# Kernel optimization log

Measured on AMD Instinct MI355X. Metric: run time of the kernel, lower is better.

The kernel has to match this reference:

```python
import jax, jax.numpy as jnp
import numpy as np

NUM_BITS_ACTS = 8
NUM_BITS_PARAMS = 8
NUM_BITS_ACCUM = 32


def quantized_range(num_bits):
    # distiller-style signed range: [-2^(n-1), 2^(n-1)-1]
    n = 2.0 ** num_bits
    return -n / 2.0, n / 2.0 - 1.0


def sym_scale(num_bits, sat_abs):
    # scale = (2^(n-1)-1) / max_abs
    return (2.0 ** (num_bits - 1) - 1.0) / sat_abs


def quant_clamp(t, scale, qmin, qmax):
    return jnp.clip(jnp.round(t * scale), qmin, qmax)


def setup_inputs() -> dict:
    key = jax.random.key(0)
    kx, kw = jax.random.split(key)
    x = jax.random.normal(kx, (8192, 4096), dtype=jnp.float32)
    W = jax.random.normal(kw, (4096, 4096), dtype=jnp.float32)  # [out, in]
    return {"x": x, "W": W}


def reference(x, W):
    acts_min, acts_max = quantized_range(NUM_BITS_ACTS)
    params_min, params_max = quantized_range(NUM_BITS_PARAMS)
    accum_min, accum_max = quantized_range(NUM_BITS_ACCUM)

    # __init__: quantize weights once (symmetric, max-abs)
    w_scale = sym_scale(NUM_BITS_PARAMS, jnp.max(jnp.abs(W)))
    W_q = quant_clamp(W, w_scale, params_min, params_max)

    # pre_quantized_forward: input scale from max-abs, quantize-clamp input
    in_scale = sym_scale(NUM_BITS_ACTS, jnp.max(jnp.abs(x)))
    x_q = quant_clamp(x, in_scale, acts_min, acts_max)

    # wrapped Linear in integer domain, clamp to accumulator range
    accum = jnp.clip(x_q @ W_q.T, accum_min, accum_max)  # [8192, 4096]

    # post_quantized_forward: requantize accumulator to output range
    accum_scale = in_scale * w_scale
    accum_max_abs = jnp.max(jnp.abs(accum))
    y_f_max_abs = accum_max_abs / accum_scale
    out_scale = sym_scale(NUM_BITS_ACTS, y_f_max_abs)
    requant_scale = out_scale / accum_scale

    out_q = quant_clamp(accum, requant_scale, acts_min, acts_max)
    out_f = out_q / out_scale  # dequantize
    return out_f
```

## Files before the change

kernel.cpp:

```cpp
#include <hip/hip_runtime.h>
#include <stdint.h>


using i32x4 = __attribute__((ext_vector_type(4))) int;

#define M_DIM 8192
#define N_DIM 4096
#define K_DIM 4096

#define BM 128
#define BN 128
#define BK 128

__global__ void k_init(unsigned* sc) {
    sc[0] = 0u;
    sc[1] = 0u;
    sc[2] = 0u;
}

__global__ __launch_bounds__(256) void k_absmax(const float4* __restrict__ src, int n4,
                                                unsigned* __restrict__ out) {
    unsigned m = 0;
    int stride = gridDim.x * blockDim.x;
    for (int i = blockIdx.x * blockDim.x + threadIdx.x; i < n4; i += stride) {
        float4 v = src[i];
        unsigned a = __float_as_uint(v.x) & 0x7fffffffu;
        unsigned b = __float_as_uint(v.y) & 0x7fffffffu;
        unsigned c = __float_as_uint(v.z) & 0x7fffffffu;
        unsigned d = __float_as_uint(v.w) & 0x7fffffffu;
        m = max(m, max(max(a, b), max(c, d)));
    }
    for (int off = 32; off; off >>= 1)
        m = max(m, (unsigned)__shfl_xor((int)m, off));
    __shared__ unsigned wm[4];
    int ln = threadIdx.x & 63, wv = threadIdx.x >> 6;
    if (ln == 0) wm[wv] = m;
    __syncthreads();
    if (threadIdx.x == 0)
        atomicMax(out, max(max(wm[0], wm[1]), max(wm[2], wm[3])));
}

__global__ __launch_bounds__(256) void k_quant(const float4* __restrict__ src,
                                               unsigned* __restrict__ dst, int n4,
                                               const unsigned* __restrict__ maxbits) {
    float scale = 127.0f / __uint_as_float(*maxbits);
    int stride = gridDim.x * blockDim.x;
    for (int i = blockIdx.x * blockDim.x + threadIdx.x; i < n4; i += stride) {
        float4 v = src[i];
        int q0 = min(127, max(-128, (int)rintf(v.x * scale)));
        int q1 = min(127, max(-128, (int)rintf(v.y * scale)));
        int q2 = min(127, max(-128, (int)rintf(v.z * scale)));
        int q3 = min(127, max(-128, (int)rintf(v.w * scale)));
        dst[i] = (unsigned)(q0 & 0xff) | ((unsigned)(q1 & 0xff) << 8) |
                 ((unsigned)(q2 & 0xff) << 16) | ((unsigned)(q3 & 0xff) << 24);
    }
}

__global__ __launch_bounds__(256) void k_gemm(const char* __restrict__ Aq,
                                              const char* __restrict__ Bq,
                                              int* __restrict__ C,
                                              unsigned* __restrict__ maxAcc) {
    __shared__ char lA[BM * BK];
    __shared__ char lB[BN * BK];

    const int bx = blockIdx.x;
    const int by = blockIdx.y;
    const int t  = threadIdx.x;
    const int ln = t & 63;
    const int wv = t >> 6;
    const int wr  = wv >> 1;
    const int wcl = wv & 1;
    const int lr = ln & 15;
    const int lk = ln >> 4;

    i32x4 acc[4][4];
#pragma unroll
    for (int i = 0; i < 4; ++i)
#pragma unroll
        for (int j = 0; j < 4; ++j) acc[i][j] = (i32x4)(0);

    const size_t arow0 = (size_t)by * BM;
    const size_t brow0 = (size_t)bx * BN;

    for (int ks = 0; ks < K_DIM / BK; ++ks) {
        const int k0 = ks * BK;
#pragma unroll
        for (int it = 0; it < 4; ++it) {
            const int chunkBase = it * 256 + (wv << 6);
            const int chunk = chunkBase + ln;
            const int row = chunk >> 3;
            const int gc = (chunk & 7) ^ (row & 7);
            const char* ga = Aq + ((arow0 + row) << 12) + k0 + (gc << 4);
            __builtin_amdgcn_global_load_lds(
                (const __attribute__((address_space(1))) void*)ga,
                (__attribute__((address_space(3))) void*)(lA + chunkBase * 16), 16, 0, 0);
            const char* gb = Bq + ((brow0 + row) << 12) + k0 + (gc << 4);
            __builtin_amdgcn_global_load_lds(
                (const __attribute__((address_space(1))) void*)gb,
                (__attribute__((address_space(3))) void*)(lB + chunkBase * 16), 16, 0, 0);
        }
        __syncthreads();

#pragma unroll
        for (int h = 0; h < 2; ++h) {
            i32x4 af[4], bf[4];
#pragma unroll
            for (int mi = 0; mi < 4; ++mi) {
                const int row = (wr << 6) + (mi << 4) + lr;
                const int sc = ((h << 2) + lk) ^ (row & 7);
                af[mi] = *(const i32x4*)(lA + row * BK + (sc << 4));
            }
#pragma unroll
            for (int ni = 0; ni < 4; ++ni) {
                const int row = (wcl << 6) + (ni << 4) + lr;
                const int sc = ((h << 2) + lk) ^ (row & 7);
                bf[ni] = *(const i32x4*)(lB + row * BK + (sc << 4));
            }
#pragma unroll
            for (int mi = 0; mi < 4; ++mi)
#pragma unroll
                for (int ni = 0; ni < 4; ++ni)
                    acc[mi][ni] = __builtin_amdgcn_mfma_i32_16x16x64_i8(
                        af[mi], bf[ni], acc[mi][ni], 0, 0, 0);
        }
        __syncthreads();
    }

    int amax = 0;
#pragma unroll
    for (int mi = 0; mi < 4; ++mi) {
#pragma unroll
        for (int ni = 0; ni < 4; ++ni) {
            const int row0 = (int)arow0 + (wr << 6) + (mi << 4) + (lk << 2);
            const int col  = (int)brow0 + (wcl << 6) + (ni << 4) + lr;
            i32x4 v = acc[mi][ni];
#pragma unroll
            for (int j = 0; j < 4; ++j) {
                C[(size_t)(row0 + j) * N_DIM + col] = v[j];
                int a = v[j] < 0 ? -v[j] : v[j];
                amax = max(amax, a);
            }
        }
    }
    for (int off = 32; off; off >>= 1)
        amax = max(amax, __shfl_xor(amax, off));
    __shared__ int wmax[4];
    if (ln == 0) wmax[wv] = amax;
    __syncthreads();
    if (t == 0)
        atomicMax(maxAcc, (unsigned)max(max(wmax[0], wmax[1]), max(wmax[2], wmax[3])));
}

__global__ __launch_bounds__(256) void k_requant(int4* __restrict__ buf, int n4,
                                                 const unsigned* __restrict__ sc) {
    const float maxX = __uint_as_float(sc[0]);
    const float maxW = __uint_as_float(sc[1]);
    const float maxA = (float)(int)sc[2];
    const float in_scale = 127.0f / maxX;
    const float w_scale  = 127.0f / maxW;
    const float accum_scale = in_scale * w_scale;
    const float requant = 127.0f / maxA;
    const float out_scale = requant * accum_scale;
    int stride = gridDim.x * blockDim.x;
    for (int i = blockIdx.x * blockDim.x + threadIdx.x; i < n4; i += stride) {
        int4 v = buf[i];
        float4 o;
        o.x = fminf(127.f, fmaxf(-128.f, rintf((float)v.x * requant))) / out_scale;
        o.y = fminf(127.f, fmaxf(-128.f, rintf((float)v.y * requant))) / out_scale;
        o.z = fminf(127.f, fmaxf(-128.f, rintf((float)v.z * requant))) / out_scale;
        o.w = fminf(127.f, fmaxf(-128.f, rintf((float)v.w * requant))) / out_scale;
        ((float4*)buf)[i] = o;
    }
}

extern "C" void kernel_launch(void* const* d_in, const int* in_sizes, int n_in,
                              void* d_out, int out_size, void* d_ws, size_t ws_size,
                              hipStream_t stream) {
    const float* x = (const float*)d_in[0];
    const float* W = (const float*)d_in[1];

    unsigned* sc = (unsigned*)d_ws;
    char* xq = (char*)d_ws + 256;
    char* wq = xq + (size_t)M_DIM * K_DIM;

    k_init<<<1, 1, 0, stream>>>(sc);
    k_absmax<<<2048, 256, 0, stream>>>((const float4*)x, M_DIM * K_DIM / 4, sc + 0);
    k_absmax<<<1024, 256, 0, stream>>>((const float4*)W, N_DIM * K_DIM / 4, sc + 1);
    k_quant<<<2048, 256, 0, stream>>>((const float4*)x, (unsigned*)xq, M_DIM * K_DIM / 4, sc + 0);
    k_quant<<<1024, 256, 0, stream>>>((const float4*)W, (unsigned*)wq, N_DIM * K_DIM / 4, sc + 1);

    dim3 g(N_DIM / BN, M_DIM / BM);
    k_gemm<<<g, 256, 0, stream>>>(xq, wq, (int*)d_out, sc + 2);

    k_requant<<<2048, 256, 0, stream>>>((int4*)d_out, M_DIM * N_DIM / 4, sc);
}
```

Baseline: 331.9 us.

## Rewrite int8 GEMM with 256x256 tiles and double-buffered LDS pipeline

The GEMM kernel moves from 128x128 tiles with 256 threads to 256x256 tiles with 512 threads (8 waves). It double-buffers the K tiles in 128KB of LDS and prefetches the next-but-one tile with global_load_lds between four MFMA phases. It also remaps block IDs in a swizzled order across XCDs and raises wave priority around MFMA bursts. The intent is to raise arithmetic intensity per block and hide global-load latency behind matrix math. In exchange it uses far more LDS and registers, which limits occupancy to about one block per CU, and many manual barriers add sync overhead.

```diff
diff --git a/kernel.cpp b/kernel.cpp
--- a/kernel.cpp
+++ b/kernel.cpp
@@ -8,9 +8,10 @@
 #define N_DIM 4096
 #define K_DIM 4096
 
-#define BM 128
-#define BN 128
-#define BK 128
+#define BM 256
+#define BN 256
+#define BKB 128
+#define NKT (K_DIM / BKB)
 
 __global__ void k_init(unsigned* sc) {
     sc[0] = 0u;
@@ -56,83 +57,176 @@
     }
 }
 
-__global__ __launch_bounds__(256) void k_gemm(const char* __restrict__ Aq,
-                                              const char* __restrict__ Bq,
-                                              int* __restrict__ C,
-                                              unsigned* __restrict__ maxAcc) {
-    __shared__ char lA[BM * BK];
-    __shared__ char lB[BN * BK];
-
-    const int bx = blockIdx.x;
-    const int by = blockIdx.y;
-    const int t  = threadIdx.x;
+__global__ __launch_bounds__(512, 2) void k_gemm(const char* __restrict__ Aq,
+                                                 const char* __restrict__ Bq,
+                                                 int* __restrict__ C,
+                                                 unsigned* __restrict__ maxAcc) {
+    __shared__ __align__(16) char lds[131072];
+    __shared__ int wmax[8];
+    char* lA = lds;
+    char* lB = lds + 65536;
+
+    const int t = threadIdx.x;
     const int ln = t & 63;
     const int wv = t >> 6;
-    const int wr  = wv >> 1;
-    const int wcl = wv & 1;
+    const int wr = wv >> 2;
+    const int wc = wv & 3;
     const int lr = ln & 15;
     const int lk = ln >> 4;
 
-    i32x4 acc[4][4];
-#pragma unroll
-    for (int i = 0; i < 4; ++i)
-#pragma unroll
-        for (int j = 0; j < 4; ++j) acc[i][j] = (i32x4)(0);
-
+    const int bid = blockIdx.x;
+    const int swz = (bid & 7) * 64 + (bid >> 3);
+    const int bx = swz & 15;
+    const int by = swz >> 4;
     const size_t arow0 = (size_t)by * BM;
     const size_t brow0 = (size_t)bx * BN;
 
-    for (int ks = 0; ks < K_DIM / BK; ++ks) {
-        const int k0 = ks * BK;
-#pragma unroll
-        for (int it = 0; it < 4; ++it) {
-            const int chunkBase = it * 256 + (wv << 6);
+    i32x4 acc[8][4];
+#pragma unroll
+    for (int i = 0; i < 8; ++i)
+#pragma unroll
+        for (int j = 0; j < 4; ++j) acc[i][j] = (i32x4)(0);
+
+    auto STAGE = [&](int kt, int j) {
+        const int slot = kt & 1;
+        const char* gbase = (j < 2) ? Aq : Bq;
+        char* lbase = ((j < 2) ? lA : lB) + slot * 32768 + (j & 1) * 16384;
+        const size_t grow0 = ((j < 2) ? arow0 : brow0) + (size_t)((j & 1) << 7);
+        const int k0 = kt * BKB;
+#pragma unroll
+        for (int it = 0; it < 2; ++it) {
+            const int chunkBase = it * 512 + (wv << 6);
             const int chunk = chunkBase + ln;
             const int row = chunk >> 3;
             const int gc = (chunk & 7) ^ (row & 7);
-            const char* ga = Aq + ((arow0 + row) << 12) + k0 + (gc << 4);
+            const char* g = gbase + ((grow0 + (size_t)row) << 12) + k0 + (gc << 4);
             __builtin_amdgcn_global_load_lds(
-                (const __attribute__((address_space(1))) void*)ga,
-                (__attribute__((address_space(3))) void*)(lA + chunkBase * 16), 16, 0, 0);
-            const char* gb = Bq + ((brow0 + row) << 12) + k0 + (gc << 4);
-            __builtin_amdgcn_global_load_lds(
-                (const __attribute__((address_space(1))) void*)gb,
-                (__attribute__((address_space(3))) void*)(lB + chunkBase * 16), 16, 0, 0);
+                (const __attribute__((address_space(1))) void*)g,
+                (__attribute__((address_space(3))) void*)(lbase + chunkBase * 16), 16, 0, 0);
         }
-        __syncthreads();
-
-#pragma unroll
-        for (int h = 0; h < 2; ++h) {
-            i32x4 af[4], bf[4];
-#pragma unroll
-            for (int mi = 0; mi < 4; ++mi) {
-                const int row = (wr << 6) + (mi << 4) + lr;
-                const int sc = ((h << 2) + lk) ^ (row & 7);
-                af[mi] = *(const i32x4*)(lA + row * BK + (sc << 4));
-            }
-#pragma unroll
-            for (int ni = 0; ni < 4; ++ni) {
-                const int row = (wcl << 6) + (ni << 4) + lr;
-                const int sc = ((h << 2) + lk) ^ (row & 7);
-                bf[ni] = *(const i32x4*)(lB + row * BK + (sc << 4));
-            }
-#pragma unroll
-            for (int mi = 0; mi < 4; ++mi)
-#pragma unroll
-                for (int ni = 0; ni < 4; ++ni)
+    };
+
+#pragma unroll
+    for (int h = 0; h < 8; ++h) STAGE(h >> 2, h & 3);
+    asm volatile("s_waitcnt vmcnt(8)" ::: "memory");
+    __builtin_amdgcn_s_barrier();
+    __builtin_amdgcn_sched_barrier(0);
+
+    for (int kt = 0; kt < NKT; ++kt) {
+        const int slot = kt & 1;
+        const char* sA = lA + slot * 32768;
+        const char* sB = lB + slot * 32768;
+        i32x4 a0[4][2], a4[4][2], b0[2][2], b2[2][2];
+
+#pragma unroll
+        for (int mi = 0; mi < 4; ++mi)
+#pragma unroll
+            for (int kh = 0; kh < 2; ++kh) {
+                const int r = (wr << 7) + (mi << 4) + lr;
+                const int cs = ((kh << 2) | lk) ^ (r & 7);
+                a0[mi][kh] = *(const i32x4*)(sA + r * 128 + (cs << 4));
+            }
+#pragma unroll
+        for (int ni = 0; ni < 2; ++ni)
+#pragma unroll
+            for (int kh = 0; kh < 2; ++kh) {
+                const int r = (wc << 6) + (ni << 4) + lr;
+                const int cs = ((kh << 2) | lk) ^ (r & 7);
+                b0[ni][kh] = *(const i32x4*)(sB + r * 128 + (cs << 4));
+            }
+        __builtin_amdgcn_s_barrier();
+        __builtin_amdgcn_sched_barrier(0);
+        asm volatile("s_waitcnt lgkmcnt(0)" ::: "memory");
+        __builtin_amdgcn_sched_barrier(0);
+        __builtin_amdgcn_s_setprio(1);
+#pragma unroll
+        for (int mi = 0; mi < 4; ++mi)
+#pragma unroll
+            for (int ni = 0; ni < 2; ++ni)
+#pragma unroll
+                for (int kh = 0; kh < 2; ++kh)
                     acc[mi][ni] = __builtin_amdgcn_mfma_i32_16x16x64_i8(
-                        af[mi], bf[ni], acc[mi][ni], 0, 0, 0);
-        }
-        __syncthreads();
+                        a0[mi][kh], b0[ni][kh], acc[mi][ni], 0, 0, 0);
+        __builtin_amdgcn_s_setprio(0);
+        __builtin_amdgcn_s_barrier();
+        __builtin_amdgcn_sched_barrier(0);
+
+#pragma unroll
+        for (int ni = 0; ni < 2; ++ni)
+#pragma unroll
+            for (int kh = 0; kh < 2; ++kh) {
+                const int r = (wc << 6) + ((ni + 2) << 4) + lr;
+                const int cs = ((kh << 2) | lk) ^ (r & 7);
+                b2[ni][kh] = *(const i32x4*)(sB + r * 128 + (cs << 4));
+            }
+        __builtin_amdgcn_s_barrier();
+        __builtin_amdgcn_sched_barrier(0);
+        asm volatile("s_waitcnt lgkmcnt(0)" ::: "memory");
+        __builtin_amdgcn_sched_barrier(0);
+        __builtin_amdgcn_s_setprio(1);
+#pragma unroll
+        for (int mi = 0; mi < 4; ++mi)
+#pragma unroll
+            for (int ni = 0; ni < 2; ++ni)
+#pragma unroll
+                for (int kh = 0; kh < 2; ++kh)
+                    acc[mi][ni + 2] = __builtin_amdgcn_mfma_i32_16x16x64_i8(
+                        a0[mi][kh], b2[ni][kh], acc[mi][ni + 2], 0, 0, 0);
+        __builtin_amdgcn_s_setprio(0);
+        __builtin_amdgcn_s_barrier();
+        __builtin_amdgcn_sched_barrier(0);
+
+#pragma unroll
+        for (int mi = 0; mi < 4; ++mi)
+#pragma unroll
+            for (int kh = 0; kh < 2; ++kh) {
+                const int r = (wr << 7) + ((mi + 4) << 4) + lr;
+                const int cs = ((kh << 2) | lk) ^ (r & 7);
+                a4[mi][kh] = *(const i32x4*)(sA + r * 128 + (cs << 4));
+            }
+        if (kt + 2 < NKT) { STAGE(kt + 2, 2); STAGE(kt + 2, 3); }
+        __builtin_amdgcn_s_barrier();
+        __builtin_amdgcn_sched_barrier(0);
+        asm volatile("s_waitcnt lgkmcnt(0)" ::: "memory");
+        __builtin_amdgcn_sched_barrier(0);
+        __builtin_amdgcn_s_setprio(1);
+#pragma unroll
+        for (int mi = 0; mi < 4; ++mi)
+#pragma unroll
+            for (int ni = 0; ni < 2; ++ni)
+#pragma unroll
+                for (int kh = 0; kh < 2; ++kh)
+                    acc[mi + 4][ni] = __builtin_amdgcn_mfma_i32_16x16x64_i8(
+                        a4[mi][kh], b0[ni][kh], acc[mi + 4][ni], 0, 0, 0);
+        __builtin_amdgcn_s_setprio(0);
+        __builtin_amdgcn_s_barrier();
+        __builtin_amdgcn_sched_barrier(0);
+
+        if (kt + 2 < NKT) { STAGE(kt + 2, 0); STAGE(kt + 2, 1); }
+        asm volatile("s_waitcnt vmcnt(8)" ::: "memory");
+        __builtin_amdgcn_s_barrier();
+        __builtin_amdgcn_sched_barrier(0);
+        __builtin_amdgcn_s_setprio(1);
+#pragma unroll
+        for (int mi = 0; mi < 4; ++mi)
+#pragma unroll
+            for (int ni = 0; ni < 2; ++ni)
+#pragma unroll
+                for (int kh = 0; kh < 2; ++kh)
+                    acc[mi + 4][ni + 2] = __builtin_amdgcn_mfma_i32_16x16x64_i8(
+                        a4[mi][kh], b2[ni][kh], acc[mi + 4][ni + 2], 0, 0, 0);
+        __builtin_amdgcn_s_setprio(0);
+        __builtin_amdgcn_s_barrier();
+        __builtin_amdgcn_sched_barrier(0);
     }
 
     int amax = 0;
 #pragma unroll
-    for (int mi = 0; mi < 4; ++mi) {
+    for (int mi = 0; mi < 8; ++mi) {
 #pragma unroll
         for (int ni = 0; ni < 4; ++ni) {
-            const int row0 = (int)arow0 + (wr << 6) + (mi << 4) + (lk << 2);
-            const int col  = (int)brow0 + (wcl << 6) + (ni << 4) + lr;
+            const int row0 = (int)arow0 + (wr << 7) + (mi << 4) + (lk << 2);
+            const int col  = (int)brow0 + (wc << 6) + (ni << 4) + lr;
             i32x4 v = acc[mi][ni];
 #pragma unroll
             for (int j = 0; j < 4; ++j) {
@@ -144,11 +238,14 @@
     }
     for (int off = 32; off; off >>= 1)
         amax = max(amax, __shfl_xor(amax, off));
-    __shared__ int wmax[4];
     if (ln == 0) wmax[wv] = amax;
     __syncthreads();
-    if (t == 0)
-        atomicMax(maxAcc, (unsigned)max(max(wmax[0], wmax[1]), max(wmax[2], wmax[3])));
+    if (t == 0) {
+        int m = wmax[0];
+#pragma unroll
+        for (int i = 1; i < 8; ++i) m = max(m, wmax[i]);
+        atomicMax(maxAcc, (unsigned)m);
+    }
 }
 
 __global__ __launch_bounds__(256) void k_requant(int4* __restrict__ buf, int n4,
@@ -189,8 +286,7 @@
     k_quant<<<2048, 256, 0, stream>>>((const float4*)x, (unsigned*)xq, M_DIM * K_DIM / 4, sc + 0);
     k_quant<<<1024, 256, 0, stream>>>((const float4*)W, (unsigned*)wq, N_DIM * K_DIM / 4, sc + 1);
 
-    dim3 g(N_DIM / BN, M_DIM / BM);
-    k_gemm<<<g, 256, 0, stream>>>(xq, wq, (int*)d_out, sc + 2);
+    k_gemm<<<(M_DIM / BM) * (N_DIM / BN), 512, 0, stream>>>(xq, wq, (int*)d_out, sc + 2);
 
     k_requant<<<2048, 256, 0, stream>>>((int4*)d_out, M_DIM * N_DIM / 4, sc);
 }
```

New measurement: 308.6 us. -7.0%, faster.
